# Performance work log

Hardware: AMD Instinct MI355X
Metric: run time of the kernel (lower is better)

Reference implementation:

```python
import jax, jax.numpy as jnp
import numpy as np

N = 50000
E = 400000
IN_DIM = 256
HEADS = 4
C = 64          # out_channels per head
HC = HEADS * C  # 256
OUT_DIM = 32
NEG_SLOPE = 0.2


def setup_inputs() -> dict:
    key = jax.random.key(0)
    ks = jax.random.split(key, 16)
    s = lambda fan_in: 1.0 / np.sqrt(fan_in)
    return {
        "x": jax.random.normal(ks[0], (N, IN_DIM), jnp.float32),
        "edge_index": jax.random.randint(ks[1], (2, E), 0, N, jnp.int64),
        # conv1 (lin_l == lin_r, shared)
        "W1": jax.random.normal(ks[2], (IN_DIM, HC), jnp.float32) * s(IN_DIM),
        "b1": jnp.zeros((HC,), jnp.float32),
        "att1": jax.random.normal(ks[3], (HEADS, C), jnp.float32) * s(C),
        # conv2
        "W2": jax.random.normal(ks[4], (HC, HC), jnp.float32) * s(HC),
        "b2": jnp.zeros((HC,), jnp.float32),
        "att2": jax.random.normal(ks[5], (HEADS, C), jnp.float32) * s(C),
        # post_mp: Linear(HC, C_hidden=64) -> Linear(64, OUT_DIM)
        "Wp1": jax.random.normal(ks[6], (HC, C), jnp.float32) * s(HC),
        "bp1": jnp.zeros((C,), jnp.float32),
        "Wp2": jax.random.normal(ks[7], (C, OUT_DIM), jnp.float32) * s(C),
        "bp2": jnp.zeros((OUT_DIM,), jnp.float32),
    }


def _gatv2_layer(x, src, dst, W, b, att):
    # shared lin_l == lin_r, so x_source == x_target projection
    h = (x @ W + b).reshape(-1, HEADS, C)          # [N, H, C]
    x_j = h[src]                                    # source features per edge [E, H, C]
    x_i = h[dst]                                    # target features per edge [E, H, C]
    e = jax.nn.leaky_relu(x_i + x_j, NEG_SLOPE)     # [E, H, C]
    alpha = jnp.einsum('ehc,hc->eh', e, att)        # [E, H]
    # segment softmax grouped by target node (dst)
    amax = jax.ops.segment_max(alpha, dst, num_segments=N)   # [N, H]
    ex = jnp.exp(alpha - amax[dst])
    denom = jax.ops.segment_sum(ex, dst, num_segments=N)     # [N, H]
    alpha = ex / (denom[dst] + 1e-16)
    out = jax.ops.segment_sum(x_j * alpha[:, :, None], dst, num_segments=N)  # [N, H, C]
    return out.reshape(-1, HC)


def reference(x, edge_index, W1, b1, att1, W2, b2, att2, Wp1, bp1, Wp2, bp2):
    src, dst = edge_index[0], edge_index[1]
    h = jax.nn.relu(_gatv2_layer(x, src, dst, W1, b1, att1))
    h = jax.nn.relu(_gatv2_layer(h, src, dst, W2, b2, att2))
    out = (h @ Wp1 + bp1) @ Wp2 + bp2
    return jax.nn.sigmoid(out)
```

## Files before the change

kernel.cpp:

```cpp
#include <hip/hip_runtime.h>
#include <math.h>

#define HC 256
#define NEG_SLOPE 0.2f
#define CAP 64

typedef __attribute__((ext_vector_type(2))) _Float16 h16x2;
typedef __attribute__((ext_vector_type(4))) _Float16 h16x4;
typedef __attribute__((ext_vector_type(8))) _Float16 f16x8;
typedef __attribute__((ext_vector_type(4))) float f32x4;

__device__ __forceinline__ unsigned short f2h16(float f) {
  _Float16 x = (_Float16)f;
  return __builtin_bit_cast(unsigned short, x);
}
__device__ __forceinline__ float h2f(unsigned short u) {
  _Float16 x = __builtin_bit_cast(_Float16, u);
  return (float)x;
}

__device__ __forceinline__ int detect64(const int* e) {
  int v = e[2 * (threadIdx.x & 63) + 1];
  return (__ballot(v != 0) == 0ULL) ? 1 : 0;
}

__device__ __forceinline__ int edge_val(const void* p, int is64, long long idx) {
  return is64 ? (int)((const long long*)p)[idx] : ((const int*)p)[idx];
}

__global__ __launch_bounds__(256) void prep_kernel(
    const float* __restrict__ W1, const float* __restrict__ W2,
    const float* __restrict__ Wp1, const float* __restrict__ bp1,
    const float* __restrict__ Wp2, const float* __restrict__ bp2,
    unsigned short* __restrict__ W1t, unsigned short* __restrict__ W2t,
    unsigned short* __restrict__ Wft16, float* __restrict__ bf) {
  const int b = blockIdx.x, t = threadIdx.x;
  if (b < 512) {
    int n = b & 255;
    const float* W = (b >> 8) ? W2 : W1;
    unsigned short* Wt = (b >> 8) ? W2t : W1t;
    Wt[(size_t)n * 256 + t] = f2h16(W[(size_t)t * 256 + n]);
    return;
  }
  float acc[32];
#pragma unroll
  for (int o = 0; o < 32; ++o) acc[o] = 0.f;
  for (int ll = 0; ll < 64; ++ll) {
    float w1 = Wp1[t * 64 + ll];
#pragma unroll
    for (int o = 0; o < 32; ++o) acc[o] += w1 * Wp2[ll * 32 + o];
  }
#pragma unroll
  for (int o = 0; o < 32; ++o) Wft16[o * 256 + t] = f2h16(acc[o]);
  if (t < 32) {
    float s = bp2[t];
    for (int ll = 0; ll < 64; ++ll) s += bp1[ll] * Wp2[ll * 32 + t];
    bf[t] = s;
  }
}

template <bool AF32>
__device__ __forceinline__ void gemm_body(
    const void* __restrict__ Araw, const unsigned short* __restrict__ Bt,
    const float* __restrict__ bias, unsigned short* __restrict__ C, int M,
    int orig, int nwg) {
  __shared__ __align__(16) short As[2][128 * 64];
  __shared__ __align__(16) short Bs[2][128 * 64];
  const int q = nwg >> 3, r = nwg & 7;
  const int xcd = orig & 7, pos = orig >> 3;
  const int logical = (xcd < r ? xcd * (q + 1) : r * (q + 1) + (xcd - r) * q) + pos;
  const int m0 = (logical >> 1) * 128, n0 = (logical & 1) * 128;

  const int t = threadIdx.x;
  const int l = t & 63, w = t >> 6;
  const int wr = w >> 1, wc = w & 1;
  const int l15 = l & 15, lg = l >> 4;

  const int ccs = ((t & 7) ^ ((t >> 3) & 7)) * 8;
  int rowL[4], ldsI[4];
#pragma unroll
  for (int i = 0; i < 4; ++i) {
    rowL[i] = i * 32 + (t >> 3);
    ldsI[i] = (i * 256 + t) * 8;
  }

  f32x4 acc[4][4];
#pragma unroll
  for (int m = 0; m < 4; ++m)
#pragma unroll
    for (int n = 0; n < 4; ++n) acc[m][n] = (f32x4){0.f, 0.f, 0.f, 0.f};

  uint4 ra[4], rb[4];
  auto LOAD = [&](int ks) {
    int k0 = ks * 64;
#pragma unroll
    for (int i = 0; i < 4; ++i) {
      int ar = m0 + rowL[i];
      ar = (ar < M) ? ar : (M - 1);
      if (AF32) {
        const float* A = (const float*)Araw;
        float4 fa = *(const float4*)(A + (size_t)ar * 256 + k0 + ccs);
        float4 fb = *(const float4*)(A + (size_t)ar * 256 + k0 + ccs + 4);
        ra[i].x = f2h16(fa.x) | ((unsigned)f2h16(fa.y) << 16);
        ra[i].y = f2h16(fa.z) | ((unsigned)f2h16(fa.w) << 16);
        ra[i].z = f2h16(fb.x) | ((unsigned)f2h16(fb.y) << 16);
        ra[i].w = f2h16(fb.z) | ((unsigned)f2h16(fb.w) << 16);
      } else {
        const unsigned short* A = (const unsigned short*)Araw;
        ra[i] = *(const uint4*)(A + (size_t)ar * 256 + k0 + ccs);
      }
      rb[i] = *(const uint4*)(Bt + (size_t)(n0 + rowL[i]) * 256 + k0 + ccs);
    }
  };
  auto WRITE = [&](int buf) {
#pragma unroll
    for (int i = 0; i < 4; ++i) {
      *(uint4*)&As[buf][ldsI[i]] = ra[i];
      *(uint4*)&Bs[buf][ldsI[i]] = rb[i];
    }
  };

  int rA[4], rB[4];
#pragma unroll
  for (int m = 0; m < 4; ++m) rA[m] = (wr * 64 + m * 16 + l15) * 64;
#pragma unroll
  for (int n = 0; n < 4; ++n) rB[n] = (wc * 64 + n * 16 + l15) * 64;
  const int swz0 = ((0 * 4 + lg) ^ (l & 7)) * 8;
  const int swz1 = ((1 * 4 + lg) ^ (l & 7)) * 8;

  LOAD(0);
  WRITE(0);
  __syncthreads();
  for (int ks = 0; ks < 4; ++ks) {
    if (ks < 3) LOAD(ks + 1);
    const int buf = ks & 1;
#pragma unroll
    for (int kk = 0; kk < 2; ++kk) {
      const int swz = kk ? swz1 : swz0;
      f16x8 a[4], b[4];
#pragma unroll
      for (int m = 0; m < 4; ++m) a[m] = *(const f16x8*)&As[buf][rA[m] + swz];
#pragma unroll
      for (int n = 0; n < 4; ++n) b[n] = *(const f16x8*)&Bs[buf][rB[n] + swz];
#pragma unroll
      for (int m = 0; m < 4; ++m)
#pragma unroll
        for (int n = 0; n < 4; ++n)
          acc[m][n] = __builtin_amdgcn_mfma_f32_16x16x32_f16(a[m], b[n], acc[m][n], 0, 0, 0);
    }
    if (ks < 3) WRITE((ks + 1) & 1);
    __syncthreads();
  }

  float bcol[4];
#pragma unroll
  for (int n = 0; n < 4; ++n) bcol[n] = bias[n0 + wc * 64 + n * 16 + l15];
#pragma unroll
  for (int m = 0; m < 4; ++m) {
    int baseRow = m0 + wr * 64 + m * 16 + lg * 4;
#pragma unroll
    for (int rr = 0; rr < 4; ++rr) {
      int row = baseRow + rr;
      if (row < M) {
#pragma unroll
        for (int n = 0; n < 4; ++n)
          C[(size_t)row * 256 + n0 + wc * 64 + n * 16 + l15] = f2h16(acc[m][n][rr] + bcol[n]);
      }
    }
  }
}

__global__ __launch_bounds__(256) void gemm1_fill_kernel(
    const float* __restrict__ x, const unsigned short* __restrict__ W1t,
    const float* __restrict__ b1, unsigned short* __restrict__ h, int M, int GB,
    const void* __restrict__ edges, int* __restrict__ cursor,
    int* __restrict__ csr_src, int E) {
  if ((int)blockIdx.x < GB) {
    gemm_body<true>((const void*)x, W1t, b1, h, M, blockIdx.x, GB);
    return;
  }
  int is64 = detect64((const int*)edges);
  int base = (blockIdx.x - GB) * 1024;
#pragma unroll
  for (int k = 0; k < 4; ++k) {
    int e = base + k * 256 + threadIdx.x;
    if (e < E) {
      int src = edge_val(edges, is64, e);
      int dst = edge_val(edges, is64, (long long)E + e);
      int p = atomicAdd(&cursor[dst], 1);
      if (p < CAP) csr_src[dst * CAP + p] = src;
    }
  }
}

__global__ __launch_bounds__(256) void gemm2_kernel(
    const unsigned short* __restrict__ A, const unsigned short* __restrict__ W2t,
    const float* __restrict__ b2, unsigned short* __restrict__ h, int M) {
  gemm_body<false>((const void*)A, W2t, b2, h, M, blockIdx.x, gridDim.x);
}

__global__ __launch_bounds__(256) void gat_fused_kernel(
    const unsigned short* __restrict__ h, const float* __restrict__ att,
    const int* __restrict__ deg, const int* __restrict__ csr_src,
    unsigned short* __restrict__ out16, int N) {
  const int wid = threadIdx.x >> 6, ln = threadIdx.x & 63;
  const int node = blockIdx.x * 4 + wid;
  if (node >= N) return;
  const float4 attv = *(const float4*)(att + ln * 4);
  const h16x2 at_lo = {(_Float16)attv.x, (_Float16)attv.y};
  const h16x2 at_hi = {(_Float16)attv.z, (_Float16)attv.w};
  const _Float16 kns = (_Float16)NEG_SLOPE;
  const h16x4 k4 = {kns, kns, kns, kns};
  const h16x4 hi4 = *(const h16x4*)(h + (size_t)node * HC + ln * 4);
  const int beg = node * CAP;
  const int cnt = min(__builtin_amdgcn_readfirstlane(deg[node]), CAP);
  const int end = beg + cnt;
  const size_t vo = (size_t)ln * 4;

  float d = 0.f;
  float4 S = make_float4(0.f, 0.f, 0.f, 0.f);

  int e0 = beg;
  for (; e0 + 8 <= end; e0 += 8) {
    h16x4 hj[8];
    float p[8];
#pragma unroll
    for (int c = 0; c < 8; ++c) {
      int j = __builtin_amdgcn_readfirstlane(csr_src[e0 + c]);
      hj[c] = *(const h16x4*)(h + (size_t)j * HC + vo);
    }
#pragma unroll
    for (int c = 0; c < 8; ++c) {
      h16x4 s4 = hi4 + hj[c];
      h16x4 l4 = __builtin_elementwise_max(s4, s4 * k4);
      float pp = __builtin_amdgcn_fdot2(l4.lo, at_lo,
                 __builtin_amdgcn_fdot2(l4.hi, at_hi, 0.f, false), false);
#pragma unroll
      for (int off = 1; off < 16; off <<= 1) pp += __shfl_xor(pp, off, 64);
      p[c] = pp;
    }
#pragma unroll
    for (int c = 0; c < 8; ++c) {
      float wgt = __expf(p[c]);
      d += wgt;
      S.x += wgt * (float)hj[c].x;
      S.y += wgt * (float)hj[c].y;
      S.z += wgt * (float)hj[c].z;
      S.w += wgt * (float)hj[c].w;
    }
  }
  if (e0 < end) {
    const int tcnt = end - e0;
    h16x4 hj[8];
#pragma unroll
    for (int c = 0; c < 8; ++c) {
      int j = __builtin_amdgcn_readfirstlane(csr_src[min(e0 + c, end - 1)]);
      hj[c] = *(const h16x4*)(h + (size_t)j * HC + vo);
    }
#pragma unroll
    for (int c = 0; c < 8; ++c) {
      if (c < tcnt) {
        h16x4 s4 = hi4 + hj[c];
        h16x4 l4 = __builtin_elementwise_max(s4, s4 * k4);
        float pp = __builtin_amdgcn_fdot2(l4.lo, at_lo,
                   __builtin_amdgcn_fdot2(l4.hi, at_hi, 0.f, false), false);
#pragma unroll
        for (int off = 1; off < 16; off <<= 1) pp += __shfl_xor(pp, off, 64);
        float wgt = __expf(pp);
        d += wgt;
        S.x += wgt * (float)hj[c].x;
        S.y += wgt * (float)hj[c].y;
        S.z += wgt * (float)hj[c].z;
        S.w += wgt * (float)hj[c].w;
      }
    }
  }

  float inv = (d > 0.f) ? (1.f / d) : 0.f;
  ushort4 ub;
  ub.x = f2h16(fmaxf(S.x * inv, 0.f));
  ub.y = f2h16(fmaxf(S.y * inv, 0.f));
  ub.z = f2h16(fmaxf(S.z * inv, 0.f));
  ub.w = f2h16(fmaxf(S.w * inv, 0.f));
  *(ushort4*)(out16 + (size_t)node * HC + vo) = ub;
}

__global__ __launch_bounds__(256) void post_kernel(
    const unsigned short* __restrict__ g, const unsigned short* __restrict__ Wft16,
    const float* __restrict__ bf, float* __restrict__ out, int M) {
  const int l = threadIdx.x & 63, w = threadIdx.x >> 6;
  const int r0 = blockIdx.x * 256 + w * 64;
  const int l15 = l & 15, lg = l >> 4;

  f16x8 bfrag[2][8];
#pragma unroll
  for (int n = 0; n < 2; ++n)
#pragma unroll
    for (int ks = 0; ks < 8; ++ks)
      bfrag[n][ks] = *(const f16x8*)(Wft16 + (size_t)(n * 16 + l15) * 256 + ks * 32 + lg * 8);

  float b0 = bf[l15], b1 = bf[16 + l15];

  f32x4 acc[4][2];
#pragma unroll
  for (int m = 0; m < 4; ++m)
#pragma unroll
    for (int n = 0; n < 2; ++n) acc[m][n] = (f32x4){0.f, 0.f, 0.f, 0.f};

#pragma unroll
  for (int m = 0; m < 4; ++m) {
    int row = r0 + m * 16 + l15;
    row = (row < M) ? row : (M - 1);
    const unsigned short* gp = g + (size_t)row * 256 + lg * 8;
#pragma unroll
    for (int ks = 0; ks < 8; ++ks) {
      f16x8 a = *(const f16x8*)(gp + ks * 32);
      acc[m][0] = __builtin_amdgcn_mfma_f32_16x16x32_f16(a, bfrag[0][ks], acc[m][0], 0, 0, 0);
      acc[m][1] = __builtin_amdgcn_mfma_f32_16x16x32_f16(a, bfrag[1][ks], acc[m][1], 0, 0, 0);
    }
  }

#pragma unroll
  for (int m = 0; m < 4; ++m) {
    int baseRow = r0 + m * 16 + lg * 4;
#pragma unroll
    for (int rr = 0; rr < 4; ++rr) {
      int row = baseRow + rr;
      if (row < M) {
        float v0 = acc[m][0][rr] + b0;
        float v1 = acc[m][1][rr] + b1;
        out[(size_t)row * 32 + l15]      = 1.f / (1.f + __expf(-v0));
        out[(size_t)row * 32 + 16 + l15] = 1.f / (1.f + __expf(-v1));
      }
    }
  }
}

extern "C" void kernel_launch(void* const* d_in, const int* in_sizes, int n_in,
                              void* d_out, int out_size, void* d_ws, size_t ws_size,
                              hipStream_t stream) {
  const float* x    = (const float*)d_in[0];
  const void*  ei   = d_in[1];
  const float* W1   = (const float*)d_in[2];
  const float* b1   = (const float*)d_in[3];
  const float* att1 = (const float*)d_in[4];
  const float* W2   = (const float*)d_in[5];
  const float* b2   = (const float*)d_in[6];
  const float* att2 = (const float*)d_in[7];
  const float* Wp1  = (const float*)d_in[8];
  const float* bp1  = (const float*)d_in[9];
  const float* Wp2  = (const float*)d_in[10];
  const float* bp2  = (const float*)d_in[11];
  const int N = in_sizes[0] / 256;
  const int E = in_sizes[1] / 2;
  float* outp = (float*)d_out;

  char* ws = (char*)d_ws;
  size_t off = 0;
  auto alloc = [&](size_t bytes) {
    char* p = ws + off;
    off = (off + bytes + 255) & ~(size_t)255;
    return p;
  };
  unsigned short* h16  = (unsigned short*)alloc((size_t)N * 256 * 2);
  unsigned short* a16  = (unsigned short*)alloc((size_t)N * 256 * 2);
  unsigned short* g16  = (unsigned short*)alloc((size_t)N * 256 * 2);
  int*   cursor   = (int*)alloc((size_t)N * 4);
  int*   csr      = (int*)alloc((size_t)N * CAP * 4);
  unsigned short* W1t = (unsigned short*)alloc(256 * 256 * 2);
  unsigned short* W2t = (unsigned short*)alloc(256 * 256 * 2);
  unsigned short* Wft16 = (unsigned short*)alloc(32 * 256 * 2);
  float* bfv      = (float*)alloc(32 * 4);

  const int CBe = (E + 1023) / 1024;
  const int mt  = (N + 127) / 128;
  const int GB  = mt * 2;

  hipMemsetAsync(cursor, 0, (size_t)N * 4, stream);
  hipLaunchKernelGGL(prep_kernel, dim3(513), dim3(256), 0, stream,
                     W1, W2, Wp1, bp1, Wp2, bp2, W1t, W2t, Wft16, bfv);
  hipLaunchKernelGGL(gemm1_fill_kernel, dim3(GB + CBe), dim3(256), 0, stream,
                     x, W1t, b1, h16, N, GB, ei, cursor, csr, E);
  hipLaunchKernelGGL(gat_fused_kernel, dim3((N + 3) / 4), dim3(256), 0, stream,
                     h16, att1, cursor, csr, a16, N);
  hipLaunchKernelGGL(gemm2_kernel, dim3(GB), dim3(256), 0, stream, a16, W2t, b2, h16, N);
  hipLaunchKernelGGL(gat_fused_kernel, dim3((N + 3) / 4), dim3(256), 0, stream,
                     h16, att2, cursor, csr, g16, N);
  hipLaunchKernelGGL(post_kernel, dim3((N + 255) / 256), dim3(256), 0, stream,
                     g16, Wft16, bfv, outp, N);
}
```

Measured before the change: 168.6 us.

## Move CSR fill into prep kernel and single-buffer GEMM shared memory

The edge-to-CSR bucketing moves out of the first GEMM launch and into the weight-prep launch, so GEMM1 runs with only GEMM blocks and the atomic fill overlaps the small weight transposes instead. The GEMM body drops its double-buffered LDS tiles for a single buffer, halving shared memory per block (64KB to 32KB) to allow more resident blocks. The price is an extra barrier per k-step and less overlap between global loads and MFMA work inside a block.

New measurement: 220.7 us. +30.9%, slower.

```diff
diff --git a/kernel.cpp b/kernel.cpp
--- a/kernel.cpp
+++ b/kernel.cpp
@@ -28,12 +28,14 @@
   return is64 ? (int)((const long long*)p)[idx] : ((const int*)p)[idx];
 }
 
-__global__ __launch_bounds__(256) void prep_kernel(
+__global__ __launch_bounds__(256) void prep_fill_kernel(
     const float* __restrict__ W1, const float* __restrict__ W2,
     const float* __restrict__ Wp1, const float* __restrict__ bp1,
     const float* __restrict__ Wp2, const float* __restrict__ bp2,
     unsigned short* __restrict__ W1t, unsigned short* __restrict__ W2t,
-    unsigned short* __restrict__ Wft16, float* __restrict__ bf) {
+    unsigned short* __restrict__ Wft16, float* __restrict__ bf,
+    const void* __restrict__ edges, int* __restrict__ cursor,
+    int* __restrict__ csr_src, int E) {
   const int b = blockIdx.x, t = threadIdx.x;
   if (b < 512) {
     int n = b & 255;
@@ -42,20 +44,35 @@
     Wt[(size_t)n * 256 + t] = f2h16(W[(size_t)t * 256 + n]);
     return;
   }
-  float acc[32];
-#pragma unroll
-  for (int o = 0; o < 32; ++o) acc[o] = 0.f;
-  for (int ll = 0; ll < 64; ++ll) {
-    float w1 = Wp1[t * 64 + ll];
-#pragma unroll
-    for (int o = 0; o < 32; ++o) acc[o] += w1 * Wp2[ll * 32 + o];
-  }
-#pragma unroll
-  for (int o = 0; o < 32; ++o) Wft16[o * 256 + t] = f2h16(acc[o]);
-  if (t < 32) {
-    float s = bp2[t];
-    for (int ll = 0; ll < 64; ++ll) s += bp1[ll] * Wp2[ll * 32 + t];
-    bf[t] = s;
+  if (b == 512) {
+    float acc[32];
+#pragma unroll
+    for (int o = 0; o < 32; ++o) acc[o] = 0.f;
+    for (int ll = 0; ll < 64; ++ll) {
+      float w1 = Wp1[t * 64 + ll];
+#pragma unroll
+      for (int o = 0; o < 32; ++o) acc[o] += w1 * Wp2[ll * 32 + o];
+    }
+#pragma unroll
+    for (int o = 0; o < 32; ++o) Wft16[o * 256 + t] = f2h16(acc[o]);
+    if (t < 32) {
+      float s = bp2[t];
+      for (int ll = 0; ll < 64; ++ll) s += bp1[ll] * Wp2[ll * 32 + t];
+      bf[t] = s;
+    }
+    return;
+  }
+  int is64 = detect64((const int*)edges);
+  int base = (b - 513) * 1024;
+#pragma unroll
+  for (int k = 0; k < 4; ++k) {
+    int e = base + k * 256 + t;
+    if (e < E) {
+      int src = edge_val(edges, is64, e);
+      int dst = edge_val(edges, is64, (long long)E + e);
+      int p = atomicAdd(&cursor[dst], 1);
+      if (p < CAP) csr_src[dst * CAP + p] = src;
+    }
   }
 }
 
@@ -64,8 +81,8 @@
     const void* __restrict__ Araw, const unsigned short* __restrict__ Bt,
     const float* __restrict__ bias, unsigned short* __restrict__ C, int M,
     int orig, int nwg) {
-  __shared__ __align__(16) short As[2][128 * 64];
-  __shared__ __align__(16) short Bs[2][128 * 64];
+  __shared__ __align__(16) short As[128 * 64];
+  __shared__ __align__(16) short Bs[128 * 64];
   const int q = nwg >> 3, r = nwg & 7;
   const int xcd = orig & 7, pos = orig >> 3;
   const int logical = (xcd < r ? xcd * (q + 1) : r * (q + 1) + (xcd - r) * q) + pos;
@@ -112,11 +129,11 @@
       rb[i] = *(const uint4*)(Bt + (size_t)(n0 + rowL[i]) * 256 + k0 + ccs);
     }
   };
-  auto WRITE = [&](int buf) {
+  auto WRITE = [&]() {
 #pragma unroll
     for (int i = 0; i < 4; ++i) {
-      *(uint4*)&As[buf][ldsI[i]] = ra[i];
-      *(uint4*)&Bs[buf][ldsI[i]] = rb[i];
+      *(uint4*)&As[ldsI[i]] = ra[i];
+      *(uint4*)&Bs[ldsI[i]] = rb[i];
     }
   };
 
@@ -129,27 +146,25 @@
   const int swz1 = ((1 * 4 + lg) ^ (l & 7)) * 8;
 
   LOAD(0);
-  WRITE(0);
-  __syncthreads();
   for (int ks = 0; ks < 4; ++ks) {
+    WRITE();
+    __syncthreads();
     if (ks < 3) LOAD(ks + 1);
-    const int buf = ks & 1;
 #pragma unroll
     for (int kk = 0; kk < 2; ++kk) {
       const int swz = kk ? swz1 : swz0;
       f16x8 a[4], b[4];
 #pragma unroll
-      for (int m = 0; m < 4; ++m) a[m] = *(const f16x8*)&As[buf][rA[m] + swz];
-#pragma unroll
-      for (int n = 0; n < 4; ++n) b[n] = *(const f16x8*)&Bs[buf][rB[n] + swz];
+      for (int m = 0; m < 4; ++m) a[m] = *(const f16x8*)&As[rA[m] + swz];
+#pragma unroll
+      for (int n = 0; n < 4; ++n) b[n] = *(const f16x8*)&Bs[rB[n] + swz];
 #pragma unroll
       for (int m = 0; m < 4; ++m)
 #pragma unroll
         for (int n = 0; n < 4; ++n)
           acc[m][n] = __builtin_amdgcn_mfma_f32_16x16x32_f16(a[m], b[n], acc[m][n], 0, 0, 0);
     }
-    if (ks < 3) WRITE((ks + 1) & 1);
-    __syncthreads();
+    if (ks < 3) __syncthreads();
   }
 
   float bcol[4];
@@ -170,27 +185,10 @@
   }
 }
 
-__global__ __launch_bounds__(256) void gemm1_fill_kernel(
+__global__ __launch_bounds__(256) void gemm1_kernel(
     const float* __restrict__ x, const unsigned short* __restrict__ W1t,
-    const float* __restrict__ b1, unsigned short* __restrict__ h, int M, int GB,
-    const void* __restrict__ edges, int* __restrict__ cursor,
-    int* __restrict__ csr_src, int E) {
-  if ((int)blockIdx.x < GB) {
-    gemm_body<true>((const void*)x, W1t, b1, h, M, blockIdx.x, GB);
-    return;
-  }
-  int is64 = detect64((const int*)edges);
-  int base = (blockIdx.x - GB) * 1024;
-#pragma unroll
-  for (int k = 0; k < 4; ++k) {
-    int e = base + k * 256 + threadIdx.x;
-    if (e < E) {
-      int src = edge_val(edges, is64, e);
-      int dst = edge_val(edges, is64, (long long)E + e);
-      int p = atomicAdd(&cursor[dst], 1);
-      if (p < CAP) csr_src[dst * CAP + p] = src;
-    }
-  }
+    const float* __restrict__ b1, unsigned short* __restrict__ h, int M) {
+  gemm_body<true>((const void*)x, W1t, b1, h, M, blockIdx.x, gridDim.x);
 }
 
 __global__ __launch_bounds__(256) void gemm2_kernel(
@@ -377,10 +375,10 @@
   const int GB  = mt * 2;
 
   hipMemsetAsync(cursor, 0, (size_t)N * 4, stream);
-  hipLaunchKernelGGL(prep_kernel, dim3(513), dim3(256), 0, stream,
-                     W1, W2, Wp1, bp1, Wp2, bp2, W1t, W2t, Wft16, bfv);
-  hipLaunchKernelGGL(gemm1_fill_kernel, dim3(GB + CBe), dim3(256), 0, stream,
-                     x, W1t, b1, h16, N, GB, ei, cursor, csr, E);
+  hipLaunchKernelGGL(prep_fill_kernel, dim3(513 + CBe), dim3(256), 0, stream,
+                     W1, W2, Wp1, bp1, Wp2, bp2, W1t, W2t, Wft16, bfv,
+                     ei, cursor, csr, E);
+  hipLaunchKernelGGL(gemm1_kernel, dim3(GB), dim3(256), 0, stream, x, W1t, b1, h16, N);
   hipLaunchKernelGGL(gat_fused_kernel, dim3((N + 3) / 4), dim3(256), 0, stream,
                      h16, att1, cursor, csr, a16, N);
   hipLaunchKernelGGL(gemm2_kernel, dim3(GB), dim3(256), 0, stream, a16, W2t, b2, h16, N);
```
